# Kernel tuning notes

Hardware: AMD Instinct MI355X
Metric: run time of the kernel (lower is better)

Reference implementation:

```python
import jax, jax.numpy as jnp
import numpy as np

NUM_ITERATIONS = 3


def squash(s):
    # Faithful to the torch code: norm taken over dim=2 of (B,1,out_units,out_size,1),
    # i.e. over the out_units axis of (B, out_units, out_size).
    mag_sq = jnp.sum(s * s, axis=1, keepdims=True)  # (B,1,out_size)
    mag = jnp.sqrt(mag_sq)
    return mag_sq / (1.0 + mag_sq) * (s / mag)


def setup_inputs() -> dict:
    key = jax.random.key(0)
    k1, k2 = jax.random.split(key)
    B, in_units, in_size = 256, 8, 1152
    out_units, out_size = 10, 16
    x = jax.random.normal(k1, (B, in_units, in_size), dtype=jnp.float32)
    W = jax.random.normal(k2, (1, in_size, out_units, out_size, in_units), dtype=jnp.float32)
    return {"x": x, "W": W}


def reference(x, W):
    B = x.shape[0]
    in_size, out_units, out_size, in_units = W.shape[1:]
    Wm = W[0]  # (in_size, out_units, out_size, in_units)
    # u_hat[b,i,j,d] = sum_u W[i,j,d,u] * x[b,u,i]
    u_hat = jnp.einsum("ijdu,bui->bijd", Wm, x)  # (B, in_size, out_units, out_size)

    b_ij = jnp.ones((in_size, out_units), dtype=x.dtype)
    v = None
    for _ in range(NUM_ITERATIONS):
        c_ij = jax.nn.softmax(b_ij, axis=0)  # softmax over in_size (dim=1 in torch)
        s_j = jnp.einsum("ij,bijd->bjd", c_ij, u_hat)  # (B, out_units, out_size)
        v = squash(s_j)
        # agreement, averaged over batch as in the torch code
        u_vj1 = jnp.einsum("bijd,bjd->ij", u_hat, v) / B
        b_ij = b_ij + u_vj1
    # torch returns v_j.squeeze(1) with trailing singleton: (B, out_units, out_size, 1)
    return v[..., None]
```

## Files before the change

### kernel.cpp

```cpp
#include <hip/hip_runtime.h>
#include <cstddef>

#define BB   256
#define UU   8
#define ISZ  1152
#define JJ   10
#define DD   16
#define JD   (JJ*DD)
#define K1   (UU*ISZ)
#define ICH  16
#define NIC  (ISZ/ICH)
#define NJH  5

#define L_ARR(it,c)  ((it)*18 + (c))
#define L_L2(it)     (54 + (it))
#define L_GO(it,g)   (57 + (it)*36 + (g))
#define L_MD(it)     (165 + (it))
#define SYNC_LINES   168
#define SYNC_U32     (SYNC_LINES*64)
#define SYNC_BYTES   (SYNC_U32*4)

typedef short v8s __attribute__((ext_vector_type(8)));
typedef float f4v __attribute__((ext_vector_type(4)));
typedef unsigned short ush;

__device__ __forceinline__ ush f2bf(float f) {
    unsigned int u = __float_as_uint(f);
    unsigned int r = (u + 0x7fffu + ((u >> 16) & 1u)) >> 16;
    return (ush)r;
}
__device__ __forceinline__ float bf2f(ush h) {
    return __uint_as_float(((unsigned int)h) << 16);
}
__device__ __forceinline__ void st_dword_sc1(float* p, float v) {
    asm volatile("global_store_dword %0, %1, off sc0 sc1" :: "v"(p), "v"(v) : "memory");
}
__device__ __forceinline__ unsigned llc_add(unsigned* p) {
    return __hip_atomic_fetch_add(p, 1u, __ATOMIC_RELAXED, __HIP_MEMORY_SCOPE_AGENT);
}

__global__ void prep_kernel(const float* __restrict__ x,
                            ush* __restrict__ xsh, ush* __restrict__ xsl,
                            ush* __restrict__ xth, ush* __restrict__ xtl,
                            float* __restrict__ b_ij) {
    __shared__ float buf[32][8][65];
    int it = blockIdx.x;
    int bt = blockIdx.y;
    int i0 = it * 64, b0 = bt * 32;
    int t = threadIdx.x, lane = t & 63, wv = t >> 6;

    int flat = bt * 18 + it;
    if (flat < 45) b_ij[flat * 256 + t] = 1.0f;

    for (int rep = 0; rep < 64; ++rep) {
        int row = rep * 4 + wv;
        int bl = row >> 3, u = row & 7;
        buf[bl][u][lane] = x[(size_t)(b0 + bl) * K1 + (size_t)u * ISZ + i0 + lane];
    }
    __syncthreads();
    {
        int bl = t >> 3, u = t & 7;
        for (int il = 0; il < 64; ++il) {
            float v = buf[bl][u][il];
            ush h = f2bf(v);
            size_t o = (size_t)(i0 + il) * 2048 + (size_t)(b0 + bl) * 8 + u;
            xsh[o] = h; xsl[o] = f2bf(v - bf2f(h));
        }
    }
    {
        int g = t >> 5, bl = t & 31;
        for (int pass = 0; pass < 64; ++pass) {
            int cu = pass * 8 + g;
            int u = cu >> 6, il = cu & 63;
            float v = buf[bl][u][il];
            ush h = f2bf(v);
            size_t o = (size_t)(u * ISZ + i0 + il) * BB + b0 + bl;
            xth[o] = h; xtl[o] = f2bf(v - bf2f(h));
        }
    }
}

__global__ __launch_bounds__(256, 2) void sgemm_red(
        const ush* __restrict__ xsh, const ush* __restrict__ xsl,
        const float* __restrict__ W, const float* __restrict__ c_tab,
        float* __restrict__ s_part, float* __restrict__ v_out,
        ush* __restrict__ vth, ush* __restrict__ vtl,
        unsigned* __restrict__ sync, int it) {
    int ic = blockIdx.x, jh = blockIdx.y;
    int fb = jh * NIC + ic;
    int j0 = jh * 2, i0 = ic * ICH;
    int t = threadIdx.x, lane = t & 63, wv = t >> 6;
    int col = lane & 15, q = lane >> 4;

    __shared__ __align__(16) ush bh_[2][16][136];
    __shared__ __align__(16) ush bl_[2][16][136];
    __shared__ float c_lds[2][ICH];
    __shared__ float smr[JD];

    if (t < 2 * ICH) {
        int cj = t >> 4, ci = t & 15;
        c_lds[cj][ci] = (it == 0) ? (1.0f / 1152.0f)
                                  : c_tab[(size_t)(j0 + cj) * ISZ + i0 + ci];
    }
    __syncthreads();

    for (int slot = t; slot < 512; slot += 256) {
        int jj = slot >> 8, rem = slot & 255, ii = rem >> 4, d = rem & 15;
        const float* wp = W + (size_t)(i0 + ii) * 1280 + (j0 + jj) * 128 + d * 8;
        float4 wa = *(const float4*)wp;
        float4 wb = *(const float4*)(wp + 4);
        float ci = c_lds[jj][ii];
        float vals[8] = { wa.x * ci, wa.y * ci, wa.z * ci, wa.w * ci,
                          wb.x * ci, wb.y * ci, wb.z * ci, wb.w * ci };
        v8s hv, lv;
#pragma unroll
        for (int u = 0; u < 8; ++u) {
            ush h = f2bf(vals[u]);
            hv[u] = (short)h;
            lv[u] = (short)f2bf(vals[u] - bf2f(h));
        }
        *(v8s*)&bh_[jj][d][ii * 8] = hv;
        *(v8s*)&bl_[jj][d][ii * 8] = lv;
    }
    __syncthreads();

    int m_base = wv * 64;
    f4v acc[4][2];
#pragma unroll
    for (int mm = 0; mm < 4; ++mm)
#pragma unroll
        for (int jj = 0; jj < 2; ++jj) acc[mm][jj] = (f4v){0.f, 0.f, 0.f, 0.f};

#pragma unroll
    for (int s = 0; s < 4; ++s) {
        v8s bh0 = *(const v8s*)&bh_[0][col][s * 32 + q * 8];
        v8s bl0 = *(const v8s*)&bl_[0][col][s * 32 + q * 8];
        v8s bh1 = *(const v8s*)&bh_[1][col][s * 32 + q * 8];
        v8s bl1 = *(const v8s*)&bl_[1][col][s * 32 + q * 8];
        size_t abase = (size_t)(i0 + s * 4 + q) * 2048;
#pragma unroll
        for (int mm = 0; mm < 4; ++mm) {
            size_t ao = abase + (size_t)(m_base + mm * 16 + col) * 8;
            v8s ah = *(const v8s*)(xsh + ao);
            v8s al = *(const v8s*)(xsl + ao);
            acc[mm][0] = __builtin_amdgcn_mfma_f32_16x16x32_bf16(ah, bh0, acc[mm][0], 0, 0, 0);
            acc[mm][0] = __builtin_amdgcn_mfma_f32_16x16x32_bf16(ah, bl0, acc[mm][0], 0, 0, 0);
            acc[mm][0] = __builtin_amdgcn_mfma_f32_16x16x32_bf16(al, bh0, acc[mm][0], 0, 0, 0);
            acc[mm][1] = __builtin_amdgcn_mfma_f32_16x16x32_bf16(ah, bh1, acc[mm][1], 0, 0, 0);
            acc[mm][1] = __builtin_amdgcn_mfma_f32_16x16x32_bf16(ah, bl1, acc[mm][1], 0, 0, 0);
            acc[mm][1] = __builtin_amdgcn_mfma_f32_16x16x32_bf16(al, bh1, acc[mm][1], 0, 0, 0);
        }
    }
#pragma unroll
    for (int mm = 0; mm < 4; ++mm)
#pragma unroll
        for (int jj = 0; jj < 2; ++jj)
#pragma unroll
            for (int r = 0; r < 4; ++r)
                st_dword_sc1(&s_part[((size_t)(m_base + mm * 16 + q * 4 + r) * NIC + ic) * JD
                                     + (j0 + jj) * DD + col], acc[mm][jj][r]);

    asm volatile("s_waitcnt vmcnt(0)" ::: "memory");
    __syncthreads();
    if (t == 0) {
        unsigned old = llc_add(&sync[L_ARR(it, fb % 18) * 64]);
        if (old == 19) {
            unsigned o2 = llc_add(&sync[L_L2(it) * 64]);
            if (o2 == 17) {
                for (int g = 0; g < 36; ++g)
                    __hip_atomic_store(&sync[L_GO(it, g) * 64], 1u,
                                       __ATOMIC_RELAXED, __HIP_MEMORY_SCOPE_AGENT);
            }
        }
    }
    if (fb >= BB) return;

    if (t == 0) {
        while (__hip_atomic_load(&sync[L_GO(it, fb % 36) * 64], __ATOMIC_RELAXED,
                                 __HIP_MEMORY_SCOPE_AGENT) == 0u) {
            __builtin_amdgcn_s_sleep(32);
        }
    }
    __syncthreads();

    int b = fb;
    if (t < JD) {
        const float* sp0 = s_part + (size_t)b * NIC * JD + t;
        float s = 0.f;
        float tmp[12];
#pragma unroll
        for (int c = 0; c < 6; ++c) {
#pragma unroll
            for (int u = 0; u < 12; ++u)
                asm volatile("global_load_dword %0, %1, off sc0 sc1"
                             : "=v"(tmp[u])
                             : "v"(sp0 + (size_t)(c * 12 + u) * JD));
            asm volatile("s_waitcnt vmcnt(0)" ::: "memory");
            __builtin_amdgcn_sched_barrier(0);
#pragma unroll
            for (int u = 0; u < 12; ++u) s += tmp[u];
        }
        smr[t] = s;
    }
    __syncthreads();
    if (t < JD) {
        int d = t & 15;
        float msq = 0.f;
#pragma unroll
        for (int j = 0; j < JJ; ++j) { float xx = smr[j * DD + d]; msq += xx * xx; }
        float val = msq / (1.f + msq) * smr[t] * rsqrtf(msq);
        if (it == 2) {
            v_out[(size_t)b * JD + t] = val;
        } else {
            ush h = f2bf(val);
            vth[(size_t)t * BB + b] = h;
            vtl[(size_t)t * BB + b] = f2bf(val - bf2f(h));
        }
    }
}

__global__ __launch_bounds__(256) void mgemm_agree(
        const ush* __restrict__ Ah, const ush* __restrict__ Al,
        const ush* __restrict__ Bh, const ush* __restrict__ Bl,
        const float* __restrict__ W, float* __restrict__ b_ij,
        float* __restrict__ c_tab, unsigned* __restrict__ sync, int it) {
    int wv = threadIdx.x >> 6, lane = threadIdx.x & 63;
    int col = lane & 15, q = lane >> 4;
    int w = blockIdx.x * 4 + wv;
    int mt = w / 288, nt2 = w % 288;
    int m0 = mt * 16;
#pragma unroll
    for (int rep = 0; rep < 2; ++rep) {
        int nt = nt2 * 2 + rep;
        int n0 = nt * 16;
        size_t aoff = (size_t)(m0 + col) * BB + q * 8;
        size_t boff = (size_t)(n0 + col) * BB + q * 8;
        f4v acc = {0.f, 0.f, 0.f, 0.f};
#pragma unroll
        for (int s = 0; s < BB / 32; ++s) {
            v8s ah = *(const v8s*)(Ah + aoff);
            v8s al = *(const v8s*)(Al + aoff);
            v8s bh = *(const v8s*)(Bh + boff);
            v8s bl = *(const v8s*)(Bl + boff);
            acc = __builtin_amdgcn_mfma_f32_16x16x32_bf16(ah, bh, acc, 0, 0, 0);
            acc = __builtin_amdgcn_mfma_f32_16x16x32_bf16(ah, bl, acc, 0, 0, 0);
            acc = __builtin_amdgcn_mfma_f32_16x16x32_bf16(al, bh, acc, 0, 0, 0);
            aoff += 32; boff += 32;
        }
        int u = nt / 72;
        int i = (nt % 72) * 16 + col;
        const float* Wp = W + (size_t)i * 1280 + mt * 128 + q * 32 + u;
        float p = Wp[0] * acc[0] + Wp[8] * acc[1] + Wp[16] * acc[2] + Wp[24] * acc[3];
        p += __shfl_xor(p, 16, 64);
        p += __shfl_xor(p, 32, 64);
        if (q == 0) atomicAdd(&b_ij[(size_t)mt * ISZ + i], p * (1.0f / 256.0f));
    }

    __shared__ unsigned lastf;
    asm volatile("s_waitcnt vmcnt(0)" ::: "memory");
    __syncthreads();
    if (threadIdx.x == 0) {
        unsigned old = llc_add(&sync[L_MD(it) * 64]);
        lastf = (old == 719u);
    }
    __syncthreads();
    if (lastf) {
        for (int j = wv; j < JJ; j += 4) {
            const float* bp = b_ij + (size_t)j * ISZ;
            float vals[18];
#pragma unroll
            for (int k = 0; k < 18; ++k) vals[k] = bp[lane + 64 * k];
            float m = -1e30f;
#pragma unroll
            for (int k = 0; k < 18; ++k) m = fmaxf(m, vals[k]);
#pragma unroll
            for (int off = 32; off; off >>= 1) m = fmaxf(m, __shfl_xor(m, off, 64));
            float ssum = 0.f;
#pragma unroll
            for (int k = 0; k < 18; ++k) ssum += __expf(vals[k] - m);
#pragma unroll
            for (int off = 32; off; off >>= 1) ssum += __shfl_xor(ssum, off, 64);
            float inv = 1.f / ssum;
#pragma unroll
            for (int k = 0; k < 18; ++k)
                c_tab[(size_t)j * ISZ + lane + 64 * k] = __expf(vals[k] - m) * inv;
        }
    }
}

extern "C" void kernel_launch(void* const* d_in, const int* in_sizes, int n_in,
                              void* d_out, int out_size, void* d_ws, size_t ws_size,
                              hipStream_t stream) {
    const float* x = (const float*)d_in[0];
    const float* W = (const float*)d_in[1];
    float* v_out = (float*)d_out;

    unsigned* sync = (unsigned*)d_ws;
    float* b_ij  = (float*)d_ws + SYNC_U32;
    float* c_tab = b_ij + ISZ * JJ;
    float* s_part = c_tab + ISZ * JJ;
    ush* xsh = (ush*)(s_part + (size_t)BB * NIC * JD);
    ush* xsl = xsh + (size_t)ISZ * 2048;
    ush* xth = xsl + (size_t)ISZ * 2048;
    ush* xtl = xth + (size_t)K1 * BB;
    ush* vth = xtl + (size_t)K1 * BB;
    ush* vtl = vth + (size_t)JD * BB;

    hipMemsetAsync(d_ws, 0, SYNC_BYTES, stream);
    hipLaunchKernelGGL(prep_kernel, dim3(18, 8), dim3(256), 0, stream,
                       x, xsh, xsl, xth, xtl, b_ij);
    for (int it = 0; it < 3; ++it) {
        hipLaunchKernelGGL(sgemm_red, dim3(NIC, NJH), dim3(256), 0, stream,
                           xsh, xsl, W, c_tab, s_part, v_out, vth, vtl, sync, it);
        if (it < 2) {
            hipLaunchKernelGGL(mgemm_agree, dim3(720), dim3(256), 0, stream,
                               vth, vtl, xth, xtl, W, b_ij, c_tab, sync, it);
        }
    }
}
```

Measured before the change: 182.6 us.

## Replace partial-sum buffer with atomic accumulation and double grid sizes

```diff
diff --git a/kernel.cpp b/kernel.cpp
--- a/kernel.cpp
+++ b/kernel.cpp
@@ -12,11 +12,11 @@
 #define NIC  (ISZ/ICH)
 #define NJH  5
 
-#define L_ARR(it,c)  ((it)*18 + (c))
-#define L_L2(it)     (54 + (it))
-#define L_GO(it,g)   (57 + (it)*36 + (g))
-#define L_MD(it)     (165 + (it))
-#define SYNC_LINES   168
+#define L_ARR(it,c)  ((it)*36 + (c))
+#define L_L2(it)     (108 + (it))
+#define L_GO(it,g)   (111 + (it)*36 + (g))
+#define L_MD(it)     (219 + (it))
+#define SYNC_LINES   222
 #define SYNC_U32     (SYNC_LINES*64)
 #define SYNC_BYTES   (SYNC_U32*4)
 
@@ -83,11 +83,11 @@
 __global__ __launch_bounds__(256, 2) void sgemm_red(
         const ush* __restrict__ xsh, const ush* __restrict__ xsl,
         const float* __restrict__ W, const float* __restrict__ c_tab,
-        float* __restrict__ s_part, float* __restrict__ v_out,
+        float* __restrict__ s_acc, float* __restrict__ v_out,
         ush* __restrict__ vth, ush* __restrict__ vtl,
         unsigned* __restrict__ sync, int it) {
-    int ic = blockIdx.x, jh = blockIdx.y;
-    int fb = jh * NIC + ic;
+    int ic = blockIdx.x, jh = blockIdx.y, z = blockIdx.z;
+    int fb = (z * NJH + jh) * NIC + ic;
     int j0 = jh * 2, i0 = ic * ICH;
     int t = threadIdx.x, lane = t & 63, wv = t >> 6;
     int col = lane & 15, q = lane >> 4;
@@ -124,10 +124,10 @@
     }
     __syncthreads();
 
-    int m_base = wv * 64;
-    f4v acc[4][2];
-#pragma unroll
-    for (int mm = 0; mm < 4; ++mm)
+    int m_base = z * 128 + wv * 32;
+    f4v acc[2][2];
+#pragma unroll
+    for (int mm = 0; mm < 2; ++mm)
 #pragma unroll
         for (int jj = 0; jj < 2; ++jj) acc[mm][jj] = (f4v){0.f, 0.f, 0.f, 0.f};
 
@@ -139,7 +139,7 @@
         v8s bl1 = *(const v8s*)&bl_[1][col][s * 32 + q * 8];
         size_t abase = (size_t)(i0 + s * 4 + q) * 2048;
 #pragma unroll
-        for (int mm = 0; mm < 4; ++mm) {
+        for (int mm = 0; mm < 2; ++mm) {
             size_t ao = abase + (size_t)(m_base + mm * 16 + col) * 8;
             v8s ah = *(const v8s*)(xsh + ao);
             v8s al = *(const v8s*)(xsl + ao);
@@ -152,21 +152,21 @@
         }
     }
 #pragma unroll
-    for (int mm = 0; mm < 4; ++mm)
+    for (int mm = 0; mm < 2; ++mm)
 #pragma unroll
         for (int jj = 0; jj < 2; ++jj)
 #pragma unroll
             for (int r = 0; r < 4; ++r)
-                st_dword_sc1(&s_part[((size_t)(m_base + mm * 16 + q * 4 + r) * NIC + ic) * JD
-                                     + (j0 + jj) * DD + col], acc[mm][jj][r]);
+                atomicAdd(&s_acc[(size_t)(m_base + mm * 16 + q * 4 + r) * JD
+                                 + (j0 + jj) * DD + col], acc[mm][jj][r]);
 
     asm volatile("s_waitcnt vmcnt(0)" ::: "memory");
     __syncthreads();
     if (t == 0) {
-        unsigned old = llc_add(&sync[L_ARR(it, fb % 18) * 64]);
+        unsigned old = llc_add(&sync[L_ARR(it, fb % 36) * 64]);
         if (old == 19) {
             unsigned o2 = llc_add(&sync[L_L2(it) * 64]);
-            if (o2 == 17) {
+            if (o2 == 35) {
                 for (int g = 0; g < 36; ++g)
                     __hip_atomic_store(&sync[L_GO(it, g) * 64], 1u,
                                        __ATOMIC_RELAXED, __HIP_MEMORY_SCOPE_AGENT);
@@ -178,29 +178,18 @@
     if (t == 0) {
         while (__hip_atomic_load(&sync[L_GO(it, fb % 36) * 64], __ATOMIC_RELAXED,
                                  __HIP_MEMORY_SCOPE_AGENT) == 0u) {
-            __builtin_amdgcn_s_sleep(32);
+            __builtin_amdgcn_s_sleep(16);
         }
     }
     __syncthreads();
 
     int b = fb;
     if (t < JD) {
-        const float* sp0 = s_part + (size_t)b * NIC * JD + t;
-        float s = 0.f;
-        float tmp[12];
-#pragma unroll
-        for (int c = 0; c < 6; ++c) {
-#pragma unroll
-            for (int u = 0; u < 12; ++u)
-                asm volatile("global_load_dword %0, %1, off sc0 sc1"
-                             : "=v"(tmp[u])
-                             : "v"(sp0 + (size_t)(c * 12 + u) * JD));
-            asm volatile("s_waitcnt vmcnt(0)" ::: "memory");
-            __builtin_amdgcn_sched_barrier(0);
-#pragma unroll
-            for (int u = 0; u < 12; ++u) s += tmp[u];
-        }
-        smr[t] = s;
+        float sv;
+        asm volatile("global_load_dword %0, %1, off sc0 sc1\n\ts_waitcnt vmcnt(0)"
+                     : "=v"(sv) : "v"(s_acc + (size_t)b * JD + t));
+        smr[t] = sv;
+        if (it < 2) st_dword_sc1(&s_acc[(size_t)b * JD + t], 0.f);
     }
     __syncthreads();
     if (t < JD) {
@@ -227,12 +216,9 @@
     int wv = threadIdx.x >> 6, lane = threadIdx.x & 63;
     int col = lane & 15, q = lane >> 4;
     int w = blockIdx.x * 4 + wv;
-    int mt = w / 288, nt2 = w % 288;
-    int m0 = mt * 16;
-#pragma unroll
-    for (int rep = 0; rep < 2; ++rep) {
-        int nt = nt2 * 2 + rep;
-        int n0 = nt * 16;
+    int mt = w / 576, nt = w % 576;
+    int m0 = mt * 16, n0 = nt * 16;
+    {
         size_t aoff = (size_t)(m0 + col) * BB + q * 8;
         size_t boff = (size_t)(n0 + col) * BB + q * 8;
         f4v acc = {0.f, 0.f, 0.f, 0.f};
@@ -261,7 +247,7 @@
     __syncthreads();
     if (threadIdx.x == 0) {
         unsigned old = llc_add(&sync[L_MD(it) * 64]);
-        lastf = (old == 719u);
+        lastf = (old == 1439u);
     }
     __syncthreads();
     if (lastf) {
@@ -296,24 +282,24 @@
     float* v_out = (float*)d_out;
 
     unsigned* sync = (unsigned*)d_ws;
-    float* b_ij  = (float*)d_ws + SYNC_U32;
+    float* s_acc = (float*)d_ws + SYNC_U32;
+    float* b_ij  = s_acc + BB * JD;
     float* c_tab = b_ij + ISZ * JJ;
-    float* s_part = c_tab + ISZ * JJ;
-    ush* xsh = (ush*)(s_part + (size_t)BB * NIC * JD);
+    ush* xsh = (ush*)(c_tab + ISZ * JJ);
     ush* xsl = xsh + (size_t)ISZ * 2048;
     ush* xth = xsl + (size_t)ISZ * 2048;
     ush* xtl = xth + (size_t)K1 * BB;
     ush* vth = xtl + (size_t)K1 * BB;
     ush* vtl = vth + (size_t)JD * BB;
 
-    hipMemsetAsync(d_ws, 0, SYNC_BYTES, stream);
+    hipMemsetAsync(d_ws, 0, SYNC_BYTES + BB * JD * 4, stream);
     hipLaunchKernelGGL(prep_kernel, dim3(18, 8), dim3(256), 0, stream,
                        x, xsh, xsl, xth, xtl, b_ij);
     for (int it = 0; it < 3; ++it) {
-        hipLaunchKernelGGL(sgemm_red, dim3(NIC, NJH), dim3(256), 0, stream,
-                           xsh, xsl, W, c_tab, s_part, v_out, vth, vtl, sync, it);
+        hipLaunchKernelGGL(sgemm_red, dim3(NIC, NJH, 2), dim3(256), 0, stream,
+                           xsh, xsl, W, c_tab, s_acc, v_out, vth, vtl, sync, it);
         if (it < 2) {
-            hipLaunchKernelGGL(mgemm_agree, dim3(720), dim3(256), 0, stream,
+            hipLaunchKernelGGL(mgemm_agree, dim3(1440), dim3(256), 0, stream,
                                vth, vtl, xth, xtl, W, b_ij, c_tab, sync, it);
         }
     }
```

After: 200.2 us. +9.6%, slower.
